# Kernel optimization log

Measured on AMD Instinct MI355X. Metric: run time of the kernel, lower is better.

Reference implementation:

```python
import jax, jax.numpy as jnp
import numpy as np

BN_EPS = 1e-5


def setup_inputs() -> dict:
    key = jax.random.key(0)
    k1, k2, k3 = jax.random.split(key, 3)
    B, Fin, N, Fout, k = 8, 64, 4096, 128, 16
    x = jax.random.normal(k1, (B, Fin, N), dtype=jnp.float32)
    # 1x1 conv weight [Fout, 2*Fin] and bias [Fout]
    W = jax.random.normal(k2, (Fout, 2 * Fin), dtype=jnp.float32) * (1.0 / np.sqrt(2 * Fin))
    b = jax.random.normal(k3, (Fout,), dtype=jnp.float32) * 0.01
    gamma = jnp.ones((Fout,), dtype=jnp.float32)
    beta = jnp.zeros((Fout,), dtype=jnp.float32)
    return {"x": x, "W": W, "b": b, "gamma": gamma, "beta": beta, "k": k}


def reference(x, W, b, gamma, beta, k):
    # x: [B, Fin, N]
    B, Fin, N = x.shape
    xt = jnp.transpose(x, (0, 2, 1))  # [B, N, Fin]
    # pairwise squared distances [B, N, N]
    sq = jnp.sum(xt * xt, axis=-1)  # [B, N]
    dist = sq[:, :, None] + sq[:, None, :] - 2.0 * jnp.einsum("bnf,bmf->bnm", xt, xt)
    # k nearest neighbours excluding self (smallest dist is self ~ 0)
    _, idx = jax.lax.top_k(-dist, k + 1)  # [B, N, k+1]
    idx = idx[:, :, 1:]  # [B, N, k]
    # gather neighbour features: [B, N, k, Fin]
    neigh = jax.vmap(lambda pts, ids: pts[ids])(xt, idx)
    central = xt[:, :, None, :]  # [B, N, 1, Fin]
    edge = jnp.concatenate(
        [jnp.broadcast_to(central, neigh.shape), neigh - central], axis=-1
    )  # [B, N, k, 2*Fin]
    # 1x1 conv == channel contraction
    y = jnp.einsum("bnkc,oc->bnko", edge, W) + b  # [B, N, k, Fout]
    # BatchNorm2d (training-mode batch stats over B, N, k per channel)
    mean = jnp.mean(y, axis=(0, 1, 2))
    var = jnp.var(y, axis=(0, 1, 2))
    y = (y - mean) * jax.lax.rsqrt(var + BN_EPS) * gamma + beta
    y = jax.nn.relu(y)
    # max over k neighbours -> [B, Fout, N]
    out = jnp.max(y, axis=2)  # [B, N, Fout]
    return jnp.transpose(out, (0, 2, 1))
```

## Files before the change

kernel.cpp:

```cpp
#include <hip/hip_runtime.h>
#include <hip/hip_bf16.h>

#define NPTS 4096
#define FIN  64
#define FOUT 128
#define KNB  16
#define BATCH 8
#define BN_EPS 1e-5f
#define FINF 1e30f

#define OFF_SQ     (0)
#define OFF_IDX    (OFF_SQ + BATCH*NPTS*4)
#define OFF_PAIRS  (OFF_IDX + BATCH*NPTS*KNB*4)
#define OFF_UBAR   (OFF_PAIRS + BATCH*NPTS*32*8)
#define OFF_VT     (OFF_UBAR + BATCH*NPTS*FOUT*4)
#define OFF_GSUM   (OFF_VT + BATCH*NPTS*FOUT*4)
#define OFF_GSUMSQ (OFF_GSUM + FOUT*4)
#define OFF_AC     (OFF_GSUMSQ + FOUT*4)

__global__ __launch_bounds__(256) void sq_kernel(const float* __restrict__ x, float* __restrict__ sq){
  int bn = blockIdx.x*256 + threadIdx.x;
  int b = bn >> 12, n = bn & (NPTS-1);
  const float* xp = x + (size_t)b*FIN*NPTS + n;
  float s = 0.f;
  #pragma unroll
  for (int f=0; f<FIN; ++f){ float v = xp[(size_t)f*NPTS]; s = fmaf(v,v,s); }
  sq[bn] = s;
}

__global__ __launch_bounds__(256) void uv_kernel(const float* __restrict__ x, const float* __restrict__ W,
                                                 const float* __restrict__ bias,
                                                 float* __restrict__ ubar, float* __restrict__ vt){
  const int t = threadIdx.x, l = t & 63;
  const int w = __builtin_amdgcn_readfirstlane(t >> 6);
  const int bid = blockIdx.x;
  const int b = bid & 7, grp = bid >> 3;
  const int n = grp*64 + l;
  const float* xp = x + (size_t)b*FIN*NPTS + n;
  float xc[FIN];
  #pragma unroll
  for (int f=0; f<FIN; ++f) xc[f] = xp[(size_t)f*NPTS];
  const size_t bn = (size_t)b*NPTS + n;
  float* up = ubar + bn*FOUT;
  float* vp = vt   + bn*FOUT;
  for (int o = w*32; o < w*32+32; ++o){
    const float* wr = W + o*2*FIN;
    float a1=0.f, a2=0.f;
    #pragma unroll
    for (int f=0; f<FIN; ++f){ a1 = fmaf(wr[f], xc[f], a1); a2 = fmaf(wr[FIN+f], xc[f], a2); }
    up[o] = a1 - a2 + bias[o];
    vp[o] = a2;
  }
}

__global__ __launch_bounds__(256,3) void knn_kernel(const float* __restrict__ x, const float* __restrict__ sq,
                                                    float2* __restrict__ pairs){
  __shared__ float xt[64*64];
  __shared__ float rowf[64*68];
  __shared__ float rowsq[64];
  __shared__ float dtile[64*68];
  const int t = threadIdx.x;
  const int w = t >> 6;
  const int l = t & 63;
  const int bid = blockIdx.x;
  const int b = bid & 7;
  const int rest = bid >> 3;
  const int z = rest & 1;
  const int n0 = (rest >> 1) * 64;
  const int cbase = z * 2048;
  const float* xb = x + (size_t)b*FIN*NPTS;

  for (int j=t; j<4096; j+=256){ int row = j & 63, f = j >> 6; rowf[row*68+f] = xb[(size_t)f*NPTS + n0 + row]; }
  if (t < 64) rowsq[t] = sq[b*NPTS + n0 + t];
  __syncthreads();

  const int cl = l & 15;
  const int rl = l >> 4;
  float rsq[4]; int nself[4];
  #pragma unroll
  for (int jr=0;jr<4;++jr){ int r = w*16 + rl*4 + jr; rsq[jr] = rowsq[r]; nself[jr] = n0 + r; }

  float val[16]; int idx[16];
  #pragma unroll
  for (int q=0;q<16;++q){ val[q] = FINF; idx[q] = 0; }
  const int selrow = w*16 + (l>>2);
  const int selc   = l & 3;
  const int selbase = selrow*68 + selc;

  for (int cc=0; cc<2048; cc+=64){
    const int c0 = cbase + cc;
    __syncthreads();
    #pragma unroll
    for (int it=0; it<4; ++it){
      int i4 = it*256 + t;
      int f  = i4 >> 4;
      int c4 = (i4 & 15) << 2;
      float4 v = *(const float4*)(xb + (size_t)f*NPTS + c0 + c4);
      int fp = f ^ c4;
      xt[(c4+0)*64 + fp] = v.x;
      xt[(c4+1)*64 + fp] = v.y;
      xt[(c4+2)*64 + fp] = v.z;
      xt[(c4+3)*64 + fp] = v.w;
    }
    float csq[4];
    #pragma unroll
    for (int jc=0;jc<4;++jc) csq[jc] = sq[b*NPTS + c0 + cl*4 + jc];
    __syncthreads();

    float acc[4][4];
    #pragma unroll
    for (int jc=0;jc<4;++jc){
      #pragma unroll
      for (int jr=0;jr<4;++jr) acc[jc][jr]=0.f;
    }
    #pragma unroll
    for (int i=0;i<16;++i){
      int fp = ((i ^ cl) << 2);
      float4 xv[4], rf[4];
      #pragma unroll
      for (int jc=0;jc<4;++jc) xv[jc] = *(const float4*)&xt[(cl*4+jc)*64 + fp];
      #pragma unroll
      for (int jr=0;jr<4;++jr) rf[jr] = *(const float4*)&rowf[(w*16+rl*4+jr)*68 + i*4];
      #pragma unroll
      for (int jc=0;jc<4;++jc){
        #pragma unroll
        for (int jr=0;jr<4;++jr){
          acc[jc][jr] = fmaf(xv[jc].x, rf[jr].x, acc[jc][jr]);
          acc[jc][jr] = fmaf(xv[jc].y, rf[jr].y, acc[jc][jr]);
          acc[jc][jr] = fmaf(xv[jc].z, rf[jr].z, acc[jc][jr]);
          acc[jc][jr] = fmaf(xv[jc].w, rf[jr].w, acc[jc][jr]);
        }
      }
    }
    #pragma unroll
    for (int jr=0;jr<4;++jr){
      int c = c0 + cl*4;
      float4 dd;
      dd.x = fmaf(-2.f, acc[0][jr], rsq[jr] + csq[0]); if (c+0 == nself[jr]) dd.x = FINF;
      dd.y = fmaf(-2.f, acc[1][jr], rsq[jr] + csq[1]); if (c+1 == nself[jr]) dd.y = FINF;
      dd.z = fmaf(-2.f, acc[2][jr], rsq[jr] + csq[2]); if (c+2 == nself[jr]) dd.z = FINF;
      dd.w = fmaf(-2.f, acc[3][jr], rsq[jr] + csq[3]); if (c+3 == nself[jr]) dd.w = FINF;
      *(float4*)&dtile[(w*16 + rl*4 + jr)*68 + cl*4] = dd;
    }
    {
      float thr = val[15];
      unsigned mask = 0;
      #pragma unroll
      for (int j=15;j>=0;--j){
        float d = dtile[selbase + 4*j];
        mask = (mask << 1) | (d < thr ? 1u : 0u);
      }
      while (mask){
        int j = __builtin_ctz(mask);
        mask &= mask - 1;
        float d = dtile[selbase + 4*j];
        if (d < val[15]){
          val[15] = d; idx[15] = c0 + selc + 4*j;
          #pragma unroll
          for (int q=15;q>0;--q){
            bool s_ = val[q] < val[q-1];
            float tv = val[q], tu = val[q-1];
            val[q]   = s_ ? tu : tv;
            val[q-1] = s_ ? tv : tu;
            int iv = idx[q], iu = idx[q-1];
            idx[q]   = s_ ? iu : iv;
            idx[q-1] = s_ ? iv : iu;
          }
        }
      }
    }
  }

  float myv[4]; int myi[4];
  #pragma unroll
  for (int round=0; round<16; ++round){
    float v = val[0]; int ii = idx[0]; int src = selc;
    #pragma unroll
    for (int mm=1; mm<4; mm<<=1){
      float ov = __shfl_xor(v, mm);
      int   oi = __shfl_xor(ii, mm);
      int   os = __shfl_xor(src, mm);
      bool take = (ov < v) || (ov == v && os < src);
      v = take ? ov : v; ii = take ? oi : ii; src = take ? os : src;
    }
    if (selc == src){
      #pragma unroll
      for (int q=0;q<15;++q){ val[q]=val[q+1]; idx[q]=idx[q+1]; }
      val[15] = FINF;
    }
    if ((round & 3) == selc){ myv[round>>2] = v; myi[round>>2] = ii; }
  }
  {
    int bn = b*NPTS + n0 + selrow;
    float2* pp = pairs + (size_t)bn*32 + z*16;
    #pragma unroll
    for (int q=0;q<4;++q) pp[q*4 + selc] = make_float2(myv[q], __int_as_float(myi[q]));
  }
}

__global__ __launch_bounds__(256) void kmerge_kernel(const float2* __restrict__ pairs, int* __restrict__ idxout){
  int bn = blockIdx.x*256 + threadIdx.x;
  const float2* p = pairs + (size_t)bn*32;
  float val[16]; int idx[16];
  #pragma unroll
  for (int q=0;q<16;++q){ float2 e = p[q]; val[q] = e.x; idx[q] = __float_as_int(e.y); }
  #pragma unroll
  for (int j=16;j<32;++j){
    float2 e = p[j];
    if (e.x < val[15]){
      val[15] = e.x; idx[15] = __float_as_int(e.y);
      #pragma unroll
      for (int q=15;q>0;--q){
        bool s_ = val[q] < val[q-1];
        float tv = val[q], tu = val[q-1];
        val[q] = s_?tu:tv; val[q-1] = s_?tv:tu;
        int iv = idx[q], iu = idx[q-1];
        idx[q] = s_?iu:iv; idx[q-1] = s_?iv:iu;
      }
    }
  }
  int* op = idxout + (size_t)bn*KNB;
  #pragma unroll
  for (int q=0;q<KNB;++q) op[q] = idx[q];
}

__global__ __launch_bounds__(256) void gather_kernel(const float* __restrict__ vt, const float* __restrict__ ubar,
                                                     const int* __restrict__ idxnb, const float* __restrict__ gamma,
                                                     float* __restrict__ outsel, float* __restrict__ gsum,
                                                     float* __restrict__ gsumsq){
  __shared__ float red[2*FOUT];
  const int t = threadIdx.x;
  const int o = t & 127;
  const int h = __builtin_amdgcn_readfirstlane(t >> 7);
  const int bid = blockIdx.x;
  const int b = bid & 7;
  const int grp = bid >> 3;
  const int nb = grp*64 + h*32;
  const float gam = gamma[o];
  const float* vtb = vt + (size_t)b*NPTS*FOUT;
  float bs = 0.f, bsq = 0.f;
  for (int p=0; p<32; ++p){
    const int n = nb + p;
    const int bn = b*NPTS + n;
    const int* ip = idxnb + (size_t)bn*KNB;
    float mx = -FINF, mn = FINF, s1 = 0.f, s2 = 0.f;
    #pragma unroll
    for (int kk=0; kk<KNB; ++kk){
      int m = ip[kk];
      float v = vtb[(size_t)m*FOUT + o];
      mx = fmaxf(mx, v); mn = fminf(mn, v); s1 += v; s2 = fmaf(v, v, s2);
    }
    float c = ubar[(size_t)bn*FOUT + o];
    outsel[((size_t)b*FOUT + o)*NPTS + n] = c + (gam >= 0.f ? mx : mn);
    bs  += fmaf(16.f, c, s1);
    bsq += fmaf(16.f*c, c, fmaf(2.f*c, s1, s2));
  }
  if (h == 1){ red[o] = bs; red[FOUT+o] = bsq; }
  __syncthreads();
  if (h == 0){ atomicAdd(&gsum[o], bs + red[o]); atomicAdd(&gsumsq[o], bsq + red[FOUT+o]); }
}

__global__ void stats_kernel(const float* __restrict__ gsum, const float* __restrict__ gsumsq,
                             const float* __restrict__ gamma, const float* __restrict__ beta,
                             float* __restrict__ ac){
  int o = threadIdx.x;
  const float invM = 1.f / (float)(BATCH*NPTS*KNB);
  float mean = gsum[o] * invM;
  float var  = gsumsq[o] * invM - mean*mean;
  float r = rsqrtf(var + BN_EPS);
  float a = gamma[o] * r;
  ac[o] = a;
  ac[FOUT+o] = beta[o] - mean * a;
}

__global__ __launch_bounds__(256) void apply_kernel(float* __restrict__ out, const float* __restrict__ ac){
  int i4 = blockIdx.x*256 + threadIdx.x;
  int o = (i4 >> 10) & 127;
  float a = ac[o], c = ac[FOUT+o];
  float4* p = (float4*)out;
  float4 v = p[i4];
  v.x = fmaxf(fmaf(a, v.x, c), 0.f);
  v.y = fmaxf(fmaf(a, v.y, c), 0.f);
  v.z = fmaxf(fmaf(a, v.z, c), 0.f);
  v.w = fmaxf(fmaf(a, v.w, c), 0.f);
  p[i4] = v;
}

extern "C" void kernel_launch(void* const* d_in, const int* in_sizes, int n_in,
                              void* d_out, int out_size, void* d_ws, size_t ws_size,
                              hipStream_t stream){
  const float* x     = (const float*)d_in[0];
  const float* W     = (const float*)d_in[1];
  const float* bias  = (const float*)d_in[2];
  const float* gamma = (const float*)d_in[3];
  const float* beta  = (const float*)d_in[4];
  char* ws = (char*)d_ws;
  float*  sq     = (float*)(ws + OFF_SQ);
  int*    idxnb  = (int*)(ws + OFF_IDX);
  float2* pairs  = (float2*)(ws + OFF_PAIRS);
  float*  ubar   = (float*)(ws + OFF_UBAR);
  float*  vt     = (float*)(ws + OFF_VT);
  float*  gsum   = (float*)(ws + OFF_GSUM);
  float*  gsumsq = (float*)(ws + OFF_GSUMSQ);
  float*  ac     = (float*)(ws + OFF_AC);
  float*  out    = (float*)d_out;

  hipMemsetAsync(ws + OFF_GSUM, 0, 2*FOUT*4, stream);
  sq_kernel    <<<BATCH*NPTS/256, 256, 0, stream>>>(x, sq);
  uv_kernel    <<<BATCH*NPTS/64,  256, 0, stream>>>(x, W, bias, ubar, vt);
  knn_kernel   <<<BATCH*(NPTS/64)*2, 256, 0, stream>>>(x, sq, pairs);
  kmerge_kernel<<<BATCH*NPTS/256, 256, 0, stream>>>(pairs, idxnb);
  gather_kernel<<<BATCH*(NPTS/64), 256, 0, stream>>>(vt, ubar, idxnb, gamma, out, gsum, gsumsq);
  stats_kernel <<<1, FOUT, 0, stream>>>(gsum, gsumsq, gamma, beta, ac);
  apply_kernel <<<BATCH*FOUT*NPTS/1024, 256, 0, stream>>>(out, ac);
}
```

Measured before the change: 704.8 us.

## Fuse sq into uv kernel, reuse LDS for distance tile, raise knn occupancy

```diff
diff --git a/kernel.cpp b/kernel.cpp
--- a/kernel.cpp
+++ b/kernel.cpp
@@ -1,5 +1,4 @@
 #include <hip/hip_runtime.h>
-#include <hip/hip_bf16.h>
 
 #define NPTS 4096
 #define FIN  64
@@ -18,19 +17,10 @@
 #define OFF_GSUMSQ (OFF_GSUM + FOUT*4)
 #define OFF_AC     (OFF_GSUMSQ + FOUT*4)
 
-__global__ __launch_bounds__(256) void sq_kernel(const float* __restrict__ x, float* __restrict__ sq){
-  int bn = blockIdx.x*256 + threadIdx.x;
-  int b = bn >> 12, n = bn & (NPTS-1);
-  const float* xp = x + (size_t)b*FIN*NPTS + n;
-  float s = 0.f;
-  #pragma unroll
-  for (int f=0; f<FIN; ++f){ float v = xp[(size_t)f*NPTS]; s = fmaf(v,v,s); }
-  sq[bn] = s;
-}
-
-__global__ __launch_bounds__(256) void uv_kernel(const float* __restrict__ x, const float* __restrict__ W,
-                                                 const float* __restrict__ bias,
-                                                 float* __restrict__ ubar, float* __restrict__ vt){
+__global__ __launch_bounds__(256) void uvsq_kernel(const float* __restrict__ x, const float* __restrict__ W,
+                                                   const float* __restrict__ bias,
+                                                   float* __restrict__ ubar, float* __restrict__ vt,
+                                                   float* __restrict__ sqout){
   const int t = threadIdx.x, l = t & 63;
   const int w = __builtin_amdgcn_readfirstlane(t >> 6);
   const int bid = blockIdx.x;
@@ -38,9 +28,11 @@
   const int n = grp*64 + l;
   const float* xp = x + (size_t)b*FIN*NPTS + n;
   float xc[FIN];
-  #pragma unroll
-  for (int f=0; f<FIN; ++f) xc[f] = xp[(size_t)f*NPTS];
+  float s = 0.f;
+  #pragma unroll
+  for (int f=0; f<FIN; ++f){ xc[f] = xp[(size_t)f*NPTS]; s = fmaf(xc[f], xc[f], s); }
   const size_t bn = (size_t)b*NPTS + n;
+  if (w == 0) sqout[bn] = s;
   float* up = ubar + bn*FOUT;
   float* vp = vt   + bn*FOUT;
   for (int o = w*32; o < w*32+32; ++o){
@@ -53,12 +45,11 @@
   }
 }
 
-__global__ __launch_bounds__(256,3) void knn_kernel(const float* __restrict__ x, const float* __restrict__ sq,
+__global__ __launch_bounds__(256,4) void knn_kernel(const float* __restrict__ x, const float* __restrict__ sq,
                                                     float2* __restrict__ pairs){
   __shared__ float xt[64*64];
   __shared__ float rowf[64*68];
   __shared__ float rowsq[64];
-  __shared__ float dtile[64*68];
   const int t = threadIdx.x;
   const int w = t >> 6;
   const int l = t & 63;
@@ -68,10 +59,11 @@
   const int z = rest & 1;
   const int n0 = (rest >> 1) * 64;
   const int cbase = z * 2048;
-  const float* xb = x + (size_t)b*FIN*NPTS;
+  const float* xb  = x  + (size_t)b*FIN*NPTS;
+  const float* sqb = sq + b*NPTS;
 
   for (int j=t; j<4096; j+=256){ int row = j & 63, f = j >> 6; rowf[row*68+f] = xb[(size_t)f*NPTS + n0 + row]; }
-  if (t < 64) rowsq[t] = sq[b*NPTS + n0 + t];
+  if (t < 64) rowsq[t] = sqb[n0 + t];
   __syncthreads();
 
   const int cl = l & 15;
@@ -85,7 +77,12 @@
   for (int q=0;q<16;++q){ val[q] = FINF; idx[q] = 0; }
   const int selrow = w*16 + (l>>2);
   const int selc   = l & 3;
-  const int selbase = selrow*68 + selc;
+  const int Xs     = (8*((l>>4)&3)) ^ (4*((l>>2)&3));
+  const int sbase  = selrow*64 + selc;
+
+  int off[16];
+  #pragma unroll
+  for (int i=0;i<16;++i) off[i] = cl*1024 + 16*(i^cl);
 
   for (int cc=0; cc<2048; cc+=64){
     const int c0 = cbase + cc;
@@ -104,7 +101,7 @@
     }
     float csq[4];
     #pragma unroll
-    for (int jc=0;jc<4;++jc) csq[jc] = sq[b*NPTS + c0 + cl*4 + jc];
+    for (int jc=0;jc<4;++jc) csq[jc] = sqb[c0 + cl*4 + jc];
     __syncthreads();
 
     float acc[4][4];
@@ -115,10 +112,9 @@
     }
     #pragma unroll
     for (int i=0;i<16;++i){
-      int fp = ((i ^ cl) << 2);
       float4 xv[4], rf[4];
       #pragma unroll
-      for (int jc=0;jc<4;++jc) xv[jc] = *(const float4*)&xt[(cl*4+jc)*64 + fp];
+      for (int jc=0;jc<4;++jc) xv[jc] = *(const float4*)((const char*)xt + off[i] + jc*256);
       #pragma unroll
       for (int jr=0;jr<4;++jr) rf[jr] = *(const float4*)&rowf[(w*16+rl*4+jr)*68 + i*4];
       #pragma unroll
@@ -132,37 +128,46 @@
         }
       }
     }
+
+    float4 dres[4];
     #pragma unroll
     for (int jr=0;jr<4;++jr){
-      int c = c0 + cl*4;
+      const int c = c0 + cl*4;
       float4 dd;
       dd.x = fmaf(-2.f, acc[0][jr], rsq[jr] + csq[0]); if (c+0 == nself[jr]) dd.x = FINF;
       dd.y = fmaf(-2.f, acc[1][jr], rsq[jr] + csq[1]); if (c+1 == nself[jr]) dd.y = FINF;
       dd.z = fmaf(-2.f, acc[2][jr], rsq[jr] + csq[2]); if (c+2 == nself[jr]) dd.z = FINF;
       dd.w = fmaf(-2.f, acc[3][jr], rsq[jr] + csq[3]); if (c+3 == nself[jr]) dd.w = FINF;
-      *(float4*)&dtile[(w*16 + rl*4 + jr)*68 + cl*4] = dd;
+      dres[jr] = dd;
+    }
+    __syncthreads();
+    #pragma unroll
+    for (int jr=0;jr<4;++jr){
+      const int row = w*16 + rl*4 + jr;
+      const int X   = (8*rl) ^ (4*jr);
+      *(float4*)&xt[row*64 + ((cl*4) ^ X)] = dres[jr];
     }
     {
-      float thr = val[15];
+      const float thr = val[15];
       unsigned mask = 0;
       #pragma unroll
       for (int j=15;j>=0;--j){
-        float d = dtile[selbase + 4*j];
+        const float d = xt[sbase + ((4*j) ^ Xs)];
         mask = (mask << 1) | (d < thr ? 1u : 0u);
       }
       while (mask){
-        int j = __builtin_ctz(mask);
+        const int j = __builtin_ctz(mask);
         mask &= mask - 1;
-        float d = dtile[selbase + 4*j];
+        const float d = xt[sbase + ((4*j) ^ Xs)];
         if (d < val[15]){
           val[15] = d; idx[15] = c0 + selc + 4*j;
           #pragma unroll
           for (int q=15;q>0;--q){
-            bool s_ = val[q] < val[q-1];
-            float tv = val[q], tu = val[q-1];
+            const bool s_ = val[q] < val[q-1];
+            const float tv = val[q], tu = val[q-1];
             val[q]   = s_ ? tu : tv;
             val[q-1] = s_ ? tv : tu;
-            int iv = idx[q], iu = idx[q-1];
+            const int iv = idx[q], iu = idx[q-1];
             idx[q]   = s_ ? iu : iv;
             idx[q-1] = s_ ? iv : iu;
           }
@@ -177,10 +182,10 @@
     float v = val[0]; int ii = idx[0]; int src = selc;
     #pragma unroll
     for (int mm=1; mm<4; mm<<=1){
-      float ov = __shfl_xor(v, mm);
-      int   oi = __shfl_xor(ii, mm);
-      int   os = __shfl_xor(src, mm);
-      bool take = (ov < v) || (ov == v && os < src);
+      const float ov = __shfl_xor(v, mm);
+      const int   oi = __shfl_xor(ii, mm);
+      const int   os = __shfl_xor(src, mm);
+      const bool take = (ov < v) || (ov == v && os < src);
       v = take ? ov : v; ii = take ? oi : ii; src = take ? os : src;
     }
     if (selc == src){
@@ -191,7 +196,7 @@
     if ((round & 3) == selc){ myv[round>>2] = v; myi[round>>2] = ii; }
   }
   {
-    int bn = b*NPTS + n0 + selrow;
+    const int bn = b*NPTS + n0 + selrow;
     float2* pp = pairs + (size_t)bn*32 + z*16;
     #pragma unroll
     for (int q=0;q<4;++q) pp[q*4 + selc] = make_float2(myv[q], __int_as_float(myi[q]));
@@ -199,7 +204,7 @@
 }
 
 __global__ __launch_bounds__(256) void kmerge_kernel(const float2* __restrict__ pairs, int* __restrict__ idxout){
-  int bn = blockIdx.x*256 + threadIdx.x;
+  const int bn = blockIdx.x*256 + threadIdx.x;
   const float2* p = pairs + (size_t)bn*32;
   float val[16]; int idx[16];
   #pragma unroll
@@ -211,10 +216,10 @@
       val[15] = e.x; idx[15] = __float_as_int(e.y);
       #pragma unroll
       for (int q=15;q>0;--q){
-        bool s_ = val[q] < val[q-1];
-        float tv = val[q], tu = val[q-1];
+        const bool s_ = val[q] < val[q-1];
+        const float tv = val[q], tu = val[q-1];
         val[q] = s_?tu:tv; val[q-1] = s_?tv:tu;
-        int iv = idx[q], iu = idx[q-1];
+        const int iv = idx[q], iu = idx[q-1];
         idx[q] = s_?iu:iv; idx[q-1] = s_?iv:iu;
       }
     }
@@ -228,55 +233,57 @@
                                                      const int* __restrict__ idxnb, const float* __restrict__ gamma,
                                                      float* __restrict__ outsel, float* __restrict__ gsum,
                                                      float* __restrict__ gsumsq){
-  __shared__ float red[2*FOUT];
   const int t = threadIdx.x;
   const int o = t & 127;
   const int h = __builtin_amdgcn_readfirstlane(t >> 7);
-  const int bid = blockIdx.x;
-  const int b = bid & 7;
-  const int grp = bid >> 3;
-  const int nb = grp*64 + h*32;
+  const int b = blockIdx.x & 7;
+  const int nblk = (blockIdx.x >> 3) * 64;
   const float gam = gamma[o];
-  const float* vtb = vt + (size_t)b*NPTS*FOUT;
+  const float* vtb = vt + (size_t)b*NPTS*FOUT + o;
   float bs = 0.f, bsq = 0.f;
-  for (int p=0; p<32; ++p){
-    const int n = nb + p;
-    const int bn = b*NPTS + n;
-    const int* ip = idxnb + (size_t)bn*KNB;
-    float mx = -FINF, mn = FINF, s1 = 0.f, s2 = 0.f;
-    #pragma unroll
-    for (int kk=0; kk<KNB; ++kk){
-      int m = ip[kk];
-      float v = vtb[(size_t)m*FOUT + o];
-      mx = fmaxf(mx, v); mn = fminf(mn, v); s1 += v; s2 = fmaf(v, v, s2);
-    }
-    float c = ubar[(size_t)bn*FOUT + o];
-    outsel[((size_t)b*FOUT + o)*NPTS + n] = c + (gam >= 0.f ? mx : mn);
-    bs  += fmaf(16.f, c, s1);
-    bsq += fmaf(16.f*c, c, fmaf(2.f*c, s1, s2));
-  }
-  if (h == 1){ red[o] = bs; red[FOUT+o] = bsq; }
-  __syncthreads();
-  if (h == 0){ atomicAdd(&gsum[o], bs + red[o]); atomicAdd(&gsumsq[o], bsq + red[FOUT+o]); }
+  for (int p=0; p<8; ++p){
+    const int ng = nblk + (h*8 + p)*4;
+    float selv[4];
+    #pragma unroll
+    for (int j=0; j<4; ++j){
+      const int n  = ng + j;
+      const int bn = b*NPTS + n;
+      const int* ip = idxnb + (size_t)bn*KNB;
+      float mx = -FINF, mn = FINF, s1 = 0.f, s2 = 0.f;
+      #pragma unroll
+      for (int kk=0; kk<KNB; ++kk){
+        const int m = ip[kk];
+        const float v = vtb[(size_t)m*FOUT];
+        mx = fmaxf(mx, v); mn = fminf(mn, v); s1 += v; s2 = fmaf(v, v, s2);
+      }
+      const float c = ubar[(size_t)bn*FOUT + o];
+      selv[j] = c + (gam >= 0.f ? mx : mn);
+      bs  += fmaf(16.f, c, s1);
+      bsq += fmaf(16.f*c, c, fmaf(2.f*c, s1, s2));
+    }
+    *(float4*)&outsel[((size_t)b*FOUT + o)*NPTS + ng] = make_float4(selv[0],selv[1],selv[2],selv[3]);
+  }
+  atomicAdd(&gsum[o], bs);
+  atomicAdd(&gsumsq[o], bsq);
 }
 
 __global__ void stats_kernel(const float* __restrict__ gsum, const float* __restrict__ gsumsq,
                              const float* __restrict__ gamma, const float* __restrict__ beta,
                              float* __restrict__ ac){
-  int o = threadIdx.x;
+  const int o = threadIdx.x;
   const float invM = 1.f / (float)(BATCH*NPTS*KNB);
-  float mean = gsum[o] * invM;
-  float var  = gsumsq[o] * invM - mean*mean;
-  float r = rsqrtf(var + BN_EPS);
-  float a = gamma[o] * r;
+  const float mean = gsum[o] * invM;
+  const float var  = gsumsq[o] * invM - mean*mean;
+  const float r = rsqrtf(var + BN_EPS);
+  const float a = gamma[o] * r;
   ac[o] = a;
   ac[FOUT+o] = beta[o] - mean * a;
 }
 
 __global__ __launch_bounds__(256) void apply_kernel(float* __restrict__ out, const float* __restrict__ ac){
-  int i4 = blockIdx.x*256 + threadIdx.x;
-  int o = (i4 >> 10) & 127;
-  float a = ac[o], c = ac[FOUT+o];
+  const int i4 = blockIdx.x*256 + threadIdx.x;
+  const int o = (i4 >> 10) & 127;
+  const float a = ac[o], c = ac[FOUT+o];
   float4* p = (float4*)out;
   float4 v = p[i4];
   v.x = fmaxf(fmaf(a, v.x, c), 0.f);
@@ -306,8 +313,7 @@
   float*  out    = (float*)d_out;
 
   hipMemsetAsync(ws + OFF_GSUM, 0, 2*FOUT*4, stream);
-  sq_kernel    <<<BATCH*NPTS/256, 256, 0, stream>>>(x, sq);
-  uv_kernel    <<<BATCH*NPTS/64,  256, 0, stream>>>(x, W, bias, ubar, vt);
+  uvsq_kernel  <<<BATCH*NPTS/64, 256, 0, stream>>>(x, W, bias, ubar, vt, sq);
   knn_kernel   <<<BATCH*(NPTS/64)*2, 256, 0, stream>>>(x, sq, pairs);
   kmerge_kernel<<<BATCH*NPTS/256, 256, 0, stream>>>(pairs, idxnb);
   gather_kernel<<<BATCH*(NPTS/64), 256, 0, stream>>>(vt, ubar, idxnb, gamma, out, gsum, gsumsq);
```

After: 1.108 ms. 1.57x slower.
